# Kernel tuning notes

Hardware: AMD Instinct MI355X
Metric: run time of the kernel (lower is better)

Reference implementation:

```python
import jax, jax.numpy as jnp
import numpy as np

ALPHA = 1.0

def setup_inputs() -> dict:
    key = jax.random.key(0)
    X = jax.random.normal(key, (2048, 128), dtype=jnp.float32)
    return {"X": X}

def reference(X) -> jnp.ndarray:
    # pairwise squared L2 distances, same math as ((X[None]-X[:,None])**2).sum(-1)
    diff = X[None, :, :] - X[:, None, :]          # [N, N, F]
    d2 = jnp.sum(diff * diff, axis=-1)            # [N, N]
    # track_running_stats=True, sigma=None -> sigma^2 = alpha * mean(d2) (detached)
    sigma_square = ALPHA * jax.lax.stop_gradient(jnp.mean(d2))
    return jnp.exp(-d2 / (2.0 * sigma_square))
```

## Files before the change

### kernel.cpp

```cpp
#include <hip/hip_runtime.h>
#include <stdint.h>

#define N 2048
#define F 128
#define ALPHA 1.0f
#define PREP_BLOCKS 32

typedef __bf16 bf16x8 __attribute__((ext_vector_type(8)));
typedef float f32x4 __attribute__((ext_vector_type(4)));

static constexpr size_t WS_XS    = 0;
static constexpr size_t WS_N     = (size_t)N * F * 2;
static constexpr size_t WS_SP    = WS_N + (size_t)N * 4;
static constexpr size_t WS_NSUMP = WS_SP + PREP_BLOCKS * F * 4;

__global__ __launch_bounds__(1024) void gk_prep(const float* __restrict__ X,
                                                ushort* __restrict__ Xs,
                                                float* __restrict__ nrm,
                                                float* __restrict__ s_part,
                                                float* __restrict__ nsum_part) {
    __shared__ float s_lds[F];
    __shared__ float nw_lds[16];
    const int t = threadIdx.x;
    if (t < F) s_lds[t] = 0.f;
    __syncthreads();

    const int rowBase = blockIdx.x * 64;
    const int r    = t >> 4;
    const int kidx = t & 15;
    const int k0   = kidx * 8;
    const int row  = rowBase + r;

    const float4* px = reinterpret_cast<const float4*>(X + (size_t)row * F + k0);
    float4 v0 = px[0], v1 = px[1];
    float xv[8] = {v0.x, v0.y, v0.z, v0.w, v1.x, v1.y, v1.z, v1.w};

    uint32_t us[8];
    float xb[8];
    float ns = 0.f;
#pragma unroll
    for (int j = 0; j < 8; ++j) {
        uint32_t u = __float_as_uint(xv[j]);
        u = (u + 0x7FFFu + ((u >> 16) & 1u)) >> 16;
        us[j] = u;
        float fb = __uint_as_float(u << 16);
        xb[j] = fb;
        ns += fb * fb;
    }
    uint4 packed;
    packed.x = us[0] | (us[1] << 16);
    packed.y = us[2] | (us[3] << 16);
    packed.z = us[4] | (us[5] << 16);
    packed.w = us[6] | (us[7] << 16);
    *reinterpret_cast<uint4*>(Xs + (size_t)(row >> 4) * 2048 + kidx * 128 + (row & 15) * 8) = packed;

    float nsr = ns;
#pragma unroll
    for (int off = 1; off < 16; off <<= 1) nsr += __shfl_xor(nsr, off, 64);
    if (kidx == 0) nrm[row] = nsr;
#pragma unroll
    for (int off = 16; off < 64; off <<= 1) nsr += __shfl_xor(nsr, off, 64);
    if ((t & 63) == 0) nw_lds[t >> 6] = nsr;

#pragma unroll
    for (int j = 0; j < 8; ++j) {
        float cj = xb[j];
        cj += __shfl_xor(cj, 16, 64);
        cj += __shfl_xor(cj, 32, 64);
        if ((t & 48) == 0) atomicAdd(&s_lds[k0 + j], cj);
    }
    __syncthreads();

    if (t < F) s_part[blockIdx.x * F + t] = s_lds[t];
    if (t == 0) {
        float v = 0.f;
#pragma unroll
        for (int w = 0; w < 16; ++w) v += nw_lds[w];
        nsum_part[blockIdx.x] = v;
    }
}

__global__ __launch_bounds__(256) void gk_main(const __bf16* __restrict__ Xs,
                                               const float* __restrict__ nrm,
                                               const float* __restrict__ s_part,
                                               const float* __restrict__ nsum_part,
                                               float* __restrict__ out) {
    __shared__ float sh_scale;
    const int t = threadIdx.x;

    if (t < 64) {
        float sc0 = 0.f, sc1 = 0.f;
#pragma unroll
        for (int b = 0; b < PREP_BLOCKS; ++b) {
            sc0 += s_part[b * F + 2 * t];
            sc1 += s_part[b * F + 2 * t + 1];
        }
        float v = sc0 * sc0 + sc1 * sc1;
        float ns = (t < PREP_BLOCKS) ? nsum_part[t] : 0.f;
#pragma unroll
        for (int off = 32; off; off >>= 1) {
            v  += __shfl_xor(v, off, 64);
            ns += __shfl_xor(ns, off, 64);
        }
        if (t == 0) {
            float meand2 = 2.f * ns / (float)N - 2.f * v / ((float)N * (float)N);
            sh_scale = -1.f / (2.f * ALPHA * meand2);
        }
    }
    __syncthreads();
    const float scale = sh_scale;

    const int wave = t >> 6, lane = t & 63;
    const int quad = lane >> 4, l16 = lane & 15;

    const int row0 = blockIdx.y * 128 + wave * 32;
    const int col0 = blockIdx.x * 64;

    bf16x8 afr[2][4], bfr[4][4];
#pragma unroll
    for (int mi = 0; mi < 2; ++mi) {
        const size_t gbase = (size_t)((row0 + mi * 16) >> 4) * 2048;
#pragma unroll
        for (int kc = 0; kc < 4; ++kc)
            afr[mi][kc] = *reinterpret_cast<const bf16x8*>(
                Xs + gbase + (kc * 4 + quad) * 128 + l16 * 8);
    }
#pragma unroll
    for (int ni = 0; ni < 4; ++ni) {
        const size_t gbase = (size_t)((col0 + ni * 16) >> 4) * 2048;
#pragma unroll
        for (int kc = 0; kc < 4; ++kc)
            bfr[ni][kc] = *reinterpret_cast<const bf16x8*>(
                Xs + gbase + (kc * 4 + quad) * 128 + l16 * 8);
    }

    float nr[2][4], nc[4];
#pragma unroll
    for (int mi = 0; mi < 2; ++mi)
#pragma unroll
        for (int rg = 0; rg < 4; ++rg)
            nr[mi][rg] = nrm[row0 + mi * 16 + quad * 4 + rg];
#pragma unroll
    for (int ni = 0; ni < 4; ++ni)
        nc[ni] = nrm[col0 + ni * 16 + l16];

#pragma unroll
    for (int mi = 0; mi < 2; ++mi) {
#pragma unroll
        for (int ni = 0; ni < 4; ++ni) {
            f32x4 acc = {0.f, 0.f, 0.f, 0.f};
#pragma unroll
            for (int kc = 0; kc < 4; ++kc)
                acc = __builtin_amdgcn_mfma_f32_16x16x32_bf16(afr[mi][kc], bfr[ni][kc], acc, 0, 0, 0);
            const int col = col0 + ni * 16 + l16;
#pragma unroll
            for (int rg = 0; rg < 4; ++rg) {
                const int row = row0 + mi * 16 + quad * 4 + rg;
                float d2 = fmaxf(nr[mi][rg] + nc[ni] - 2.f * acc[rg], 0.f);
                out[(size_t)row * N + col] = __expf(scale * d2);
            }
        }
    }
}

extern "C" void kernel_launch(void* const* d_in, const int* in_sizes, int n_in,
                              void* d_out, int out_size, void* d_ws, size_t ws_size,
                              hipStream_t stream) {
    const float* X = (const float*)d_in[0];
    float* out = (float*)d_out;
    char* ws = (char*)d_ws;

    ushort* Xs     = (ushort*)(ws + WS_XS);
    float*  nrm    = (float*)(ws + WS_N);
    float*  s_part = (float*)(ws + WS_SP);
    float*  nsum_p = (float*)(ws + WS_NSUMP);

    gk_prep<<<N / 64, 1024, 0, stream>>>(X, Xs, nrm, s_part, nsum_p);

    dim3 grid(N / 64, N / 128);
    gk_main<<<grid, 256, 0, stream>>>((const __bf16*)Xs, nrm, s_part, nsum_p, out);
}
```

Baseline: 66.88 us.

## Swap MFMA operands for vectorized nontemporal stores and atomically reduce column sums

```diff
diff --git a/kernel.cpp b/kernel.cpp
--- a/kernel.cpp
+++ b/kernel.cpp
@@ -4,32 +4,32 @@
 #define N 2048
 #define F 128
 #define ALPHA 1.0f
-#define PREP_BLOCKS 32
+#define PREP_BLOCKS 128
 
 typedef __bf16 bf16x8 __attribute__((ext_vector_type(8)));
 typedef float f32x4 __attribute__((ext_vector_type(4)));
 
-static constexpr size_t WS_XS    = 0;
-static constexpr size_t WS_N     = (size_t)N * F * 2;
-static constexpr size_t WS_SP    = WS_N + (size_t)N * 4;
-static constexpr size_t WS_NSUMP = WS_SP + PREP_BLOCKS * F * 4;
+static constexpr size_t WS_XS  = 0;
+static constexpr size_t WS_N   = (size_t)N * F * 2;
+static constexpr size_t WS_SF  = WS_N + (size_t)N * 4;
+static constexpr size_t WS_NSF = WS_SF + (size_t)F * 4;
+static constexpr size_t WS_ZERO_BYTES = (size_t)F * 4 + 4;
 
-__global__ __launch_bounds__(1024) void gk_prep(const float* __restrict__ X,
-                                                ushort* __restrict__ Xs,
-                                                float* __restrict__ nrm,
-                                                float* __restrict__ s_part,
-                                                float* __restrict__ nsum_part) {
+__global__ __launch_bounds__(256) void gk_prep(const float* __restrict__ X,
+                                               ushort* __restrict__ Xs,
+                                               float* __restrict__ nrm,
+                                               float* __restrict__ s_final,
+                                               float* __restrict__ nsum_final) {
     __shared__ float s_lds[F];
-    __shared__ float nw_lds[16];
+    __shared__ float nw_lds[4];
     const int t = threadIdx.x;
     if (t < F) s_lds[t] = 0.f;
     __syncthreads();
 
-    const int rowBase = blockIdx.x * 64;
     const int r    = t >> 4;
     const int kidx = t & 15;
     const int k0   = kidx * 8;
-    const int row  = rowBase + r;
+    const int row  = blockIdx.x * 16 + r;
 
     const float4* px = reinterpret_cast<const float4*>(X + (size_t)row * F + k0);
     float4 v0 = px[0], v1 = px[1];
@@ -52,7 +52,7 @@
     packed.y = us[2] | (us[3] << 16);
     packed.z = us[4] | (us[5] << 16);
     packed.w = us[6] | (us[7] << 16);
-    *reinterpret_cast<uint4*>(Xs + (size_t)(row >> 4) * 2048 + kidx * 128 + (row & 15) * 8) = packed;
+    *reinterpret_cast<uint4*>(Xs + (size_t)blockIdx.x * 2048 + kidx * 128 + r * 8) = packed;
 
     float nsr = ns;
 #pragma unroll
@@ -71,45 +71,16 @@
     }
     __syncthreads();
 
-    if (t < F) s_part[blockIdx.x * F + t] = s_lds[t];
-    if (t == 0) {
-        float v = 0.f;
-#pragma unroll
-        for (int w = 0; w < 16; ++w) v += nw_lds[w];
-        nsum_part[blockIdx.x] = v;
-    }
+    if (t < F) atomicAdd(&s_final[t], s_lds[t]);
+    if (t == 0) atomicAdd(nsum_final, nw_lds[0] + nw_lds[1] + nw_lds[2] + nw_lds[3]);
 }
 
 __global__ __launch_bounds__(256) void gk_main(const __bf16* __restrict__ Xs,
                                                const float* __restrict__ nrm,
-                                               const float* __restrict__ s_part,
-                                               const float* __restrict__ nsum_part,
+                                               const float* __restrict__ s_final,
+                                               const float* __restrict__ nsum_final,
                                                float* __restrict__ out) {
-    __shared__ float sh_scale;
     const int t = threadIdx.x;
-
-    if (t < 64) {
-        float sc0 = 0.f, sc1 = 0.f;
-#pragma unroll
-        for (int b = 0; b < PREP_BLOCKS; ++b) {
-            sc0 += s_part[b * F + 2 * t];
-            sc1 += s_part[b * F + 2 * t + 1];
-        }
-        float v = sc0 * sc0 + sc1 * sc1;
-        float ns = (t < PREP_BLOCKS) ? nsum_part[t] : 0.f;
-#pragma unroll
-        for (int off = 32; off; off >>= 1) {
-            v  += __shfl_xor(v, off, 64);
-            ns += __shfl_xor(ns, off, 64);
-        }
-        if (t == 0) {
-            float meand2 = 2.f * ns / (float)N - 2.f * v / ((float)N * (float)N);
-            sh_scale = -1.f / (2.f * ALPHA * meand2);
-        }
-    }
-    __syncthreads();
-    const float scale = sh_scale;
-
     const int wave = t >> 6, lane = t & 63;
     const int quad = lane >> 4, l16 = lane & 15;
 
@@ -134,31 +105,39 @@
                 Xs + gbase + (kc * 4 + quad) * 128 + l16 * 8);
     }
 
-    float nr[2][4], nc[4];
+    float nr[2];
 #pragma unroll
-    for (int mi = 0; mi < 2; ++mi)
-#pragma unroll
-        for (int rg = 0; rg < 4; ++rg)
-            nr[mi][rg] = nrm[row0 + mi * 16 + quad * 4 + rg];
+    for (int mi = 0; mi < 2; ++mi) nr[mi] = nrm[row0 + mi * 16 + l16];
+    f32x4 ncv[4];
 #pragma unroll
     for (int ni = 0; ni < 4; ++ni)
-        nc[ni] = nrm[col0 + ni * 16 + l16];
+        ncv[ni] = *reinterpret_cast<const f32x4*>(nrm + col0 + ni * 16 + quad * 4);
+
+    float c0 = s_final[2 * lane], c1 = s_final[2 * lane + 1];
+    float nsum = *nsum_final;
+    float v = c0 * c0 + c1 * c1;
+#pragma unroll
+    for (int off = 32; off; off >>= 1) v += __shfl_xor(v, off, 64);
+    const float invn = 1.f / (float)N;
+    const float meand2 = 2.f * invn * (nsum - v * invn);
+    const float scale = -1.f / (2.f * ALPHA * meand2);
 
 #pragma unroll
     for (int mi = 0; mi < 2; ++mi) {
+        float* orow = out + (size_t)(row0 + mi * 16 + l16) * N + col0 + quad * 4;
 #pragma unroll
         for (int ni = 0; ni < 4; ++ni) {
             f32x4 acc = {0.f, 0.f, 0.f, 0.f};
 #pragma unroll
             for (int kc = 0; kc < 4; ++kc)
-                acc = __builtin_amdgcn_mfma_f32_16x16x32_bf16(afr[mi][kc], bfr[ni][kc], acc, 0, 0, 0);
-            const int col = col0 + ni * 16 + l16;
+                acc = __builtin_amdgcn_mfma_f32_16x16x32_bf16(bfr[ni][kc], afr[mi][kc], acc, 0, 0, 0);
+            f32x4 rv;
 #pragma unroll
             for (int rg = 0; rg < 4; ++rg) {
-                const int row = row0 + mi * 16 + quad * 4 + rg;
-                float d2 = fmaxf(nr[mi][rg] + nc[ni] - 2.f * acc[rg], 0.f);
-                out[(size_t)row * N + col] = __expf(scale * d2);
+                float d2 = fmaxf(nr[mi] + ncv[ni][rg] - 2.f * acc[rg], 0.f);
+                rv[rg] = __expf(scale * d2);
             }
+            __builtin_nontemporal_store(rv, reinterpret_cast<f32x4*>(orow + ni * 16));
         }
     }
 }
@@ -170,13 +149,14 @@
     float* out = (float*)d_out;
     char* ws = (char*)d_ws;
 
-    ushort* Xs     = (ushort*)(ws + WS_XS);
-    float*  nrm    = (float*)(ws + WS_N);
-    float*  s_part = (float*)(ws + WS_SP);
-    float*  nsum_p = (float*)(ws + WS_NSUMP);
+    ushort* Xs         = (ushort*)(ws + WS_XS);
+    float*  nrm        = (float*)(ws + WS_N);
+    float*  s_final    = (float*)(ws + WS_SF);
+    float*  nsum_final = (float*)(ws + WS_NSF);
 
-    gk_prep<<<N / 64, 1024, 0, stream>>>(X, Xs, nrm, s_part, nsum_p);
+    hipMemsetAsync(ws + WS_SF, 0, WS_ZERO_BYTES, stream);
+    gk_prep<<<PREP_BLOCKS, 256, 0, stream>>>(X, Xs, nrm, s_final, nsum_final);
 
     dim3 grid(N / 64, N / 128);
-    gk_main<<<grid, 256, 0, stream>>>((const __bf16*)Xs, nrm, s_part, nsum_p, out);
+    gk_main<<<grid, 256, 0, stream>>>((const __bf16*)Xs, nrm, s_final, nsum_final, out);
 }
```

After: 69.91 us. 1.05x slower.
